# Kernel optimization log

Hardware: AMD Instinct MI355X
Metric: run time of the kernel (lower is better)

## Reference

```python
import jax, jax.numpy as jnp
import numpy as np


def setup_inputs() -> dict:
    key = jax.random.key(0)
    k1, k2 = jax.random.split(key)
    B, V, D = 2048, 2000, 64
    # multi-hot weights in [0,1); zeros denote absent categories
    inputs = jax.random.uniform(k1, (B, V), dtype=jnp.float32)
    # embedding table, uniform(-1, 1) as in Ludwig's default initializer
    embeddings = jax.random.uniform(k2, (V, D), dtype=jnp.float32, minval=-1.0, maxval=1.0)
    return {"inputs": inputs, "embeddings": embeddings}


def reference(inputs, embeddings):
    # inputs: (B, V) float weights; embeddings: (V, D)
    V = embeddings.shape[0]
    # signed_input = sign(abs(inputs)) -> 1 where nonzero, else 0
    # multiple_hot_indexes = signed_input * arange(V)  (zeros map to row 0)
    idx = jnp.where(inputs != 0, jnp.arange(V, dtype=jnp.int32)[None, :], 0)  # (B, V)
    gathered = embeddings[idx]  # (B, V, D) — dense lookup, as in the original
    # weighted multiply + sum-reduce over the vocab axis
    out = jnp.einsum("bv,bvd->bd", inputs, gathered)  # (B, D)
    return out
```

## Files before the change

kernel.cpp:

```cpp
#include <hip/hip_runtime.h>


#define Bn 2048
#define Vn 2000
#define Dn 64
#define KCH 16
#define KBLK 128
#define MBLK 64
#define LSTR 136
#define NKS 64
#define EFRAG_FLOATS 65536

typedef __attribute__((ext_vector_type(8))) short bf16x8;
typedef __attribute__((ext_vector_type(4))) float f32x4;

__device__ inline unsigned short bf16r(float x) {
    union { float f; unsigned u; } c; c.f = x;
    return (unsigned short)((c.u + 0x8000u) >> 16);
}

__global__ __launch_bounds__(256)
void efrag_k(const float* __restrict__ E, uint4* __restrict__ ef) {
    const int ks   = blockIdx.x;
    const int ct   = threadIdx.x >> 6;
    const int lane = threadIdx.x & 63;
    const int d    = ct * 16 + (lane & 15);
    const int kb   = ks * 32 + (lane >> 4) * 8;
    unsigned short h[8];
#pragma unroll
    for (int j = 0; j < 8; ++j) {
        const int gk = kb + j;
        h[j] = (gk < Vn) ? bf16r(E[(size_t)gk * Dn + d]) : (unsigned short)0;
    }
    uint4 v;
    v.x = (unsigned)h[0] | ((unsigned)h[1] << 16);
    v.y = (unsigned)h[2] | ((unsigned)h[3] << 16);
    v.z = (unsigned)h[4] | ((unsigned)h[5] << 16);
    v.w = (unsigned)h[6] | ((unsigned)h[7] << 16);
    ef[((size_t)ks * 4 + ct) * 64 + lane] = v;
}

__global__ __launch_bounds__(256)
void embw_mfma(const float* __restrict__ A, const bf16x8* __restrict__ ef,
               float* __restrict__ part) {
    __shared__ unsigned short Al[MBLK][LSTR];

    const int t    = threadIdx.x;
    const int lane = t & 63;
    const int w    = t >> 6;
    const int kc   = blockIdx.x >> 5;
    const int mblk = blockIdx.x & 31;
    const int m0   = mblk * MBLK;
    const int k0   = kc * KBLK;

    {
        const int rs = t >> 5;
        const int c4 = t & 31;
        const int gk = k0 + c4 * 4;
        const bool real = (gk < Vn);
#pragma unroll
        for (int s = 0; s < 8; ++s) {
            const int row = s * 8 + rs;
            float4 v = make_float4(0.f, 0.f, 0.f, 0.f);
            if (real)
                v = *(const float4*)&A[(size_t)(m0 + row) * Vn + gk];
            unsigned lo = ((unsigned)bf16r(v.y) << 16) | bf16r(v.x);
            unsigned hi = ((unsigned)bf16r(v.w) << 16) | bf16r(v.z);
            *(uint2*)&Al[row][c4 * 4] = make_uint2(lo, hi);
        }
    }
    __syncthreads();

    const int fr = lane & 15;
    const int fk = (lane >> 4) * 8;
    f32x4 acc0 = {0.f,0.f,0.f,0.f}, acc1 = {0.f,0.f,0.f,0.f};
    f32x4 acc2 = {0.f,0.f,0.f,0.f}, acc3 = {0.f,0.f,0.f,0.f};

#pragma unroll
    for (int ks = 0; ks < KBLK / 32; ++ks) {
        const int ksg = kc * 4 + ks;
        const size_t eb = ((size_t)ksg * 4) * 64 + lane;
        bf16x8 af = *(const bf16x8*)&Al[w * 16 + fr][ks * 32 + fk];
        bf16x8 b0 = ef[eb +   0];
        bf16x8 b1 = ef[eb +  64];
        bf16x8 b2 = ef[eb + 128];
        bf16x8 b3 = ef[eb + 192];
        acc0 = __builtin_amdgcn_mfma_f32_16x16x32_bf16(af, b0, acc0, 0, 0, 0);
        acc1 = __builtin_amdgcn_mfma_f32_16x16x32_bf16(af, b1, acc1, 0, 0, 0);
        acc2 = __builtin_amdgcn_mfma_f32_16x16x32_bf16(af, b2, acc2, 0, 0, 0);
        acc3 = __builtin_amdgcn_mfma_f32_16x16x32_bf16(af, b3, acc3, 0, 0, 0);
    }

    float* pp = part + ((size_t)kc * Bn + m0 + w * 16 + (lane >> 4) * 4) * Dn + fr;
#pragma unroll
    for (int q = 0; q < 4; ++q) {
        pp[(size_t)q * Dn +  0] = acc0[q];
        pp[(size_t)q * Dn + 16] = acc1[q];
        pp[(size_t)q * Dn + 32] = acc2[q];
        pp[(size_t)q * Dn + 48] = acc3[q];
    }
}

__global__ __launch_bounds__(256)
void embw_reduce(const float* __restrict__ part, float* __restrict__ out) {
    const int i = blockIdx.x * 256 + threadIdx.x;
    const float4* p = (const float4*)part;
    float4 s = p[i];
#pragma unroll
    for (int c = 1; c < KCH; ++c) {
        float4 tv = p[(size_t)c * (Bn * Dn / 4) + i];
        s.x += tv.x; s.y += tv.y; s.z += tv.z; s.w += tv.w;
    }
    ((float4*)out)[i] = s;
}

extern "C" void kernel_launch(void* const* d_in, const int* in_sizes, int n_in,
                              void* d_out, int out_size, void* d_ws, size_t ws_size,
                              hipStream_t stream) {
    const float* in  = (const float*)d_in[0];
    const float* emb = (const float*)d_in[1];
    float* out = (float*)d_out;

    uint4* efrag = (uint4*)d_ws;
    float* part  = (float*)d_ws + EFRAG_FLOATS;

    efrag_k<<<NKS, 256, 0, stream>>>(emb, efrag);
    embw_mfma<<<32 * KCH, 256, 0, stream>>>(in, (const bf16x8*)efrag, part);
    embw_reduce<<<(Bn * Dn / 4) / 256, 256, 0, stream>>>(part, out);
}
```

Measured before the change: 74.28 us.

## Fuse split-K GEMM and reduction into one kernel with in-block LDS reduce

Replaces the split-K MFMA kernel plus global partial-sum reduce kernel with a single kernel where each block handles 4 batch rows over the full vocabulary. Each wave covers a quarter of K and partial results are combined in shared memory. This removes the partial buffer round trip and one launch. In exchange, MFMA tiles are only a quarter utilized and every block re-reads the full embedding fragment table from cache.

```diff
diff --git a/kernel.cpp b/kernel.cpp
--- a/kernel.cpp
+++ b/kernel.cpp
@@ -4,12 +4,8 @@
 #define Bn 2048
 #define Vn 2000
 #define Dn 64
-#define KCH 16
-#define KBLK 128
-#define MBLK 64
-#define LSTR 136
 #define NKS 64
-#define EFRAG_FLOATS 65536
+#define LSTR2 2056
 
 typedef __attribute__((ext_vector_type(8))) short bf16x8;
 typedef __attribute__((ext_vector_type(4))) float f32x4;
@@ -17,6 +13,9 @@
 __device__ inline unsigned short bf16r(float x) {
     union { float f; unsigned u; } c; c.f = x;
     return (unsigned short)((c.u + 0x8000u) >> 16);
+}
+__device__ inline unsigned pk2(float a, float b) {
+    return ((unsigned)bf16r(b) << 16) | bf16r(a);
 }
 
 __global__ __launch_bounds__(256)
@@ -41,46 +40,40 @@
 }
 
 __global__ __launch_bounds__(256)
-void embw_mfma(const float* __restrict__ A, const bf16x8* __restrict__ ef,
-               float* __restrict__ part) {
-    __shared__ unsigned short Al[MBLK][LSTR];
+void embw_fused(const float* __restrict__ A, const bf16x8* __restrict__ ef,
+                float* __restrict__ out) {
+    __shared__ unsigned short Al[4][LSTR2];
+    __shared__ float red[4][4][64];
 
     const int t    = threadIdx.x;
     const int lane = t & 63;
     const int w    = t >> 6;
-    const int kc   = blockIdx.x >> 5;
-    const int mblk = blockIdx.x & 31;
-    const int m0   = mblk * MBLK;
-    const int k0   = kc * KBLK;
+    const int r0   = blockIdx.x * 4;
 
     {
-        const int rs = t >> 5;
-        const int c4 = t & 31;
-        const int gk = k0 + c4 * 4;
-        const bool real = (gk < Vn);
-#pragma unroll
-        for (int s = 0; s < 8; ++s) {
-            const int row = s * 8 + rs;
-            float4 v = make_float4(0.f, 0.f, 0.f, 0.f);
-            if (real)
-                v = *(const float4*)&A[(size_t)(m0 + row) * Vn + gk];
-            unsigned lo = ((unsigned)bf16r(v.y) << 16) | bf16r(v.x);
-            unsigned hi = ((unsigned)bf16r(v.w) << 16) | bf16r(v.z);
-            *(uint2*)&Al[row][c4 * 4] = make_uint2(lo, hi);
+        const float* src = A + (size_t)(r0 + w) * Vn;
+#pragma unroll 1
+        for (int k4 = lane; k4 < Vn / 4; k4 += 64) {
+            float4 v = *(const float4*)&src[k4 * 4];
+            *(uint2*)&Al[w][k4 * 4] = make_uint2(pk2(v.x, v.y), pk2(v.z, v.w));
         }
+        if (lane < 24)
+            *(unsigned*)&Al[w][Vn + lane * 2] = 0u;
     }
     __syncthreads();
 
     const int fr = lane & 15;
     const int fk = (lane >> 4) * 8;
+    const unsigned short* arow = Al[fr & 3];
+
     f32x4 acc0 = {0.f,0.f,0.f,0.f}, acc1 = {0.f,0.f,0.f,0.f};
     f32x4 acc2 = {0.f,0.f,0.f,0.f}, acc3 = {0.f,0.f,0.f,0.f};
 
-#pragma unroll
-    for (int ks = 0; ks < KBLK / 32; ++ks) {
-        const int ksg = kc * 4 + ks;
-        const size_t eb = ((size_t)ksg * 4) * 64 + lane;
-        bf16x8 af = *(const bf16x8*)&Al[w * 16 + fr][ks * 32 + fk];
+#pragma unroll 4
+    for (int i = 0; i < 16; ++i) {
+        const int ks = w * 16 + i;
+        const size_t eb = (size_t)ks * 256 + lane;
+        bf16x8 af = *(const bf16x8*)&arow[ks * 32 + fk];
         bf16x8 b0 = ef[eb +   0];
         bf16x8 b1 = ef[eb +  64];
         bf16x8 b2 = ef[eb + 128];
@@ -91,27 +84,23 @@
         acc3 = __builtin_amdgcn_mfma_f32_16x16x32_bf16(af, b3, acc3, 0, 0, 0);
     }
 
-    float* pp = part + ((size_t)kc * Bn + m0 + w * 16 + (lane >> 4) * 4) * Dn + fr;
+    if (lane < 16) {
 #pragma unroll
-    for (int q = 0; q < 4; ++q) {
-        pp[(size_t)q * Dn +  0] = acc0[q];
-        pp[(size_t)q * Dn + 16] = acc1[q];
-        pp[(size_t)q * Dn + 32] = acc2[q];
-        pp[(size_t)q * Dn + 48] = acc3[q];
+        for (int q = 0; q < 4; ++q) {
+            red[w][q][ 0 + fr] = acc0[q];
+            red[w][q][16 + fr] = acc1[q];
+            red[w][q][32 + fr] = acc2[q];
+            red[w][q][48 + fr] = acc3[q];
+        }
     }
-}
-
-__global__ __launch_bounds__(256)
-void embw_reduce(const float* __restrict__ part, float* __restrict__ out) {
-    const int i = blockIdx.x * 256 + threadIdx.x;
-    const float4* p = (const float4*)part;
-    float4 s = p[i];
-#pragma unroll
-    for (int c = 1; c < KCH; ++c) {
-        float4 tv = p[(size_t)c * (Bn * Dn / 4) + i];
-        s.x += tv.x; s.y += tv.y; s.z += tv.z; s.w += tv.w;
+    __syncthreads();
+    {
+        const int row = t >> 6;
+        const int col = t & 63;
+        float s = red[0][row][col] + red[1][row][col]
+                + red[2][row][col] + red[3][row][col];
+        out[(size_t)(r0 + row) * Dn + col] = s;
     }
-    ((float4*)out)[i] = s;
 }
 
 extern "C" void kernel_launch(void* const* d_in, const int* in_sizes, int n_in,
@@ -122,9 +111,7 @@
     float* out = (float*)d_out;
 
     uint4* efrag = (uint4*)d_ws;
-    float* part  = (float*)d_ws + EFRAG_FLOATS;
 
     efrag_k<<<NKS, 256, 0, stream>>>(emb, efrag);
-    embw_mfma<<<32 * KCH, 256, 0, stream>>>(in, (const bf16x8*)efrag, part);
-    embw_reduce<<<(Bn * Dn / 4) / 256, 256, 0, stream>>>(part, out);
+    embw_fused<<<Bn / 4, 256, 0, stream>>>(in, (const bf16x8*)efrag, out);
 }
```

Result: no change. 74.71 us (+0.6%).
